# Kernel tuning notes

Measured on AMD Instinct MI355X. Metric: run time of the kernel, lower is better.

Reference implementation:

```python
import jax, jax.numpy as jnp
import numpy as np

B, CIN, H, W = 32, 64, 128, 128
HID, OUT, E, S, R = 64, 64, 8, 2, 16
TOP_K = 2
TEMP = 2.0
BN_EPS = 1e-5


def setup_inputs() -> dict:
    key = jax.random.key(0)
    ks = jax.random.split(key, 16)
    sc = lambda fan: 1.0 / np.sqrt(fan)
    h2 = 2 * HID
    return {
        "x": jax.random.normal(ks[0], (B, CIN, H, W), jnp.float32),
        "fe_w": jax.random.normal(ks[1], (HID, CIN), jnp.float32) * sc(CIN),
        "fe_b": jnp.zeros((HID,), jnp.float32),
        "s_w": jax.random.normal(ks[2], (S, OUT, HID), jnp.float32) * sc(HID),
        "s_b": jnp.zeros((S, OUT), jnp.float32),
        "e_w": jax.random.normal(ks[3], (E, OUT, HID), jnp.float32) * sc(HID),
        "e_b": jnp.zeros((E, OUT), jnp.float32),
        "g1_w": jax.random.normal(ks[4], (h2, HID), jnp.float32) * sc(HID),
        "g1_b": jnp.zeros((h2,), jnp.float32),
        "bn1_g": jnp.ones((h2,), jnp.float32),
        "bn1_b": jnp.zeros((h2,), jnp.float32),
        "ca1_w": jax.random.normal(ks[5], (h2 // R, h2), jnp.float32) * sc(h2),
        "ca1_b": jnp.zeros((h2 // R,), jnp.float32),
        "ca2_w": jax.random.normal(ks[6], (h2, h2 // R), jnp.float32) * sc(h2 // R),
        "ca2_b": jnp.zeros((h2,), jnp.float32),
        "g2_w": jax.random.normal(ks[7], (HID, h2), jnp.float32) * sc(h2),
        "g2_b": jnp.zeros((HID,), jnp.float32),
        "bn2_g": jnp.ones((HID,), jnp.float32),
        "bn2_b": jnp.zeros((HID,), jnp.float32),
        "g3_w": jax.random.normal(ks[8], (E, HID), jnp.float32) * sc(HID),
        "g3_b": jnp.zeros((E,), jnp.float32),
    }


def _gelu(v):
    return jax.nn.gelu(v, approximate=False)


def _bn_eval(v, g, b):
    # BatchNorm eval mode with running_mean=0, running_var=1
    return v * (g / np.sqrt(1.0 + BN_EPS)) + b


def reference(x, fe_w, fe_b, s_w, s_b, e_w, e_b, g1_w, g1_b, bn1_g, bn1_b,
              ca1_w, ca1_b, ca2_w, ca2_b, g2_w, g2_b, bn2_g, bn2_b, g3_w, g3_b):
    # feature extractor: 1x1 conv + GELU
    features = _gelu(jnp.einsum('bchw,oc->bohw', x, fe_w) + fe_b[None, :, None, None])

    # shared experts: mean of S expert outputs (sum / S)
    shared = _gelu(jnp.einsum('bchw,soc->bsohw', features, s_w)
                   + s_b[None, :, :, None, None]).mean(axis=1)

    # gating on globally pooled features [B, HID]
    gf = features.mean(axis=(2, 3))
    h1 = _gelu(_bn_eval(gf @ g1_w.T + g1_b, bn1_g, bn1_b))  # [B, 2*HID]
    # ChannelAttention on 1x1 spatial: avg_pool == max_pool == identity
    att = _gelu(h1 @ ca1_w.T + ca1_b) @ ca2_w.T + ca2_b
    h1 = h1 * jax.nn.sigmoid(att + att)  # avg_out + max_out are identical
    hh = _gelu(_bn_eval(h1 @ g2_w.T + g2_b, bn2_g, bn2_b))  # [B, HID]
    scores = hh @ g3_w.T + g3_b  # [B, E]

    top_vals, top_idx = jax.lax.top_k(scores, TOP_K)
    top_w = jax.nn.softmax(top_vals / TEMP, axis=1)  # [B, TOP_K]
    # dense per-(sample, expert) weights
    dense_w = jnp.zeros((x.shape[0], E), scores.dtype).at[
        jnp.arange(x.shape[0])[:, None], top_idx].add(top_w)

    # all experts on full batch, then weighted accumulate (matches original loop)
    eo = _gelu(jnp.einsum('bchw,eoc->beohw', features, e_w)
               + e_b[None, :, :, None, None])  # [B, E, OUT, H, W]
    routed = jnp.einsum('beohw,be->bohw', eo, dense_w)

    return shared + routed
```

## Files before the change

kernel.cpp:

```cpp
#include <hip/hip_runtime.h>
#include <hip/hip_bf16.h>
#include <stdint.h>

#define HW 16384

typedef __bf16 bf16_t;
typedef bf16_t bf16x8 __attribute__((ext_vector_type(8)));
typedef float f32x4 __attribute__((ext_vector_type(4)));

__device__ __forceinline__ float gelu_f(float x) {
    float t = x * fmaf(x * x, 0.044715f, 1.0f);
    float e = __builtin_amdgcn_exp2f(-2.3022083f * t);
    return x * __builtin_amdgcn_rcpf(1.0f + e);
}

__device__ __forceinline__ uint32_t pk2(float a, float b) {
    union { bf16_t h[2]; uint32_t u; } z;
    z.h[0] = (bf16_t)a; z.h[1] = (bf16_t)b;
    return z.u;
}

__device__ __forceinline__ void load16_to_lds(const float* g, float* lds) {
    __builtin_amdgcn_global_load_lds(
        (const __attribute__((address_space(1))) uint32_t*)g,
        (__attribute__((address_space(3))) uint32_t*)lds, 16, 0, 0);
}

__device__ __forceinline__ bf16x8 frag8(const float* src) {
    float4 lo = ((const float4*)src)[0];
    float4 hi = ((const float4*)src)[1];
    bf16x8 r;
    r[0] = (bf16_t)lo.x; r[1] = (bf16_t)lo.y; r[2] = (bf16_t)lo.z; r[3] = (bf16_t)lo.w;
    r[4] = (bf16_t)hi.x; r[5] = (bf16_t)hi.y; r[6] = (bf16_t)hi.z; r[7] = (bf16_t)hi.w;
    return r;
}

__device__ __forceinline__ bf16x8 frag44(const float* a, const float* b) {
    float4 lo = *(const float4*)a;
    float4 hi = *(const float4*)b;
    bf16x8 r;
    r[0] = (bf16_t)lo.x; r[1] = (bf16_t)lo.y; r[2] = (bf16_t)lo.z; r[3] = (bf16_t)lo.w;
    r[4] = (bf16_t)hi.x; r[5] = (bf16_t)hi.y; r[6] = (bf16_t)hi.z; r[7] = (bf16_t)hi.w;
    return r;
}

__global__ __launch_bounds__(256, 3)
void k1_feat(const float* __restrict__ x, const float* __restrict__ fe_w,
             const float* __restrict__ fe_b, bf16_t* __restrict__ feat,
             float* __restrict__ gf_part) {
    __shared__ float xs[3][64 * 64];
    __shared__ float gf4[4][64];

    int tid = threadIdx.x;
    int lane = tid & 63;
    int wid = tid >> 6;
    int r16 = lane & 15;
    int g = lane >> 4;
    int b = blockIdx.x >> 5;
    int ss = blockIdx.x & 31;
    int p0 = ss * 512;

    bf16x8 A[4][2];
    f32x4 bias[4];
#pragma unroll
    for (int ot = 0; ot < 4; ++ot) {
#pragma unroll
        for (int kh = 0; kh < 2; ++kh)
            A[ot][kh] = frag8(fe_w + (ot * 16 + r16) * 64 + kh * 32 + g * 8);
#pragma unroll
        for (int r = 0; r < 4; ++r) bias[ot][r] = fe_b[ot * 16 + g * 4 + r];
    }
    asm volatile("" ::: "memory");

    int j16 = lane & 15;
    int rsub = lane >> 4;

    auto STAGE = [&](int buf, int i) {
#pragma unroll
        for (int s = 0; s < 4; ++s) {
            int c0 = wid * 16 + s * 4;
            int c = c0 + rsub;
            int gch = j16 ^ (((c >> 3) & 3) << 2);
            const float* gsrc = x + (size_t)(b * 64 + c) * HW + p0 + i * 64 + gch * 4;
            load16_to_lds(gsrc, &xs[buf][c0 * 64]);
        }
    };

    float gfp[4][4] = {};
    bf16_t* featb = feat + (size_t)b * HW * 64;
    int wb = 16 * (wid ^ g) + r16;

    auto COMPUTE = [&](int buf, int i) {
        bf16x8 B0, B1;
#pragma unroll
        for (int j = 0; j < 8; ++j) {
            B0[j] = (bf16_t)xs[buf][(g * 8 + j) * 64 + wb];
            B1[j] = (bf16_t)xs[buf][(32 + g * 8 + j) * 64 + wb];
        }
        int pg = p0 + i * 64 + wid * 16 + r16;
        float vals[4][4];
#pragma unroll
        for (int ot = 0; ot < 4; ++ot) {
            f32x4 y = {0.f, 0.f, 0.f, 0.f};
            y = __builtin_amdgcn_mfma_f32_16x16x32_bf16(A[ot][0], B0, y, 0, 0, 0);
            y = __builtin_amdgcn_mfma_f32_16x16x32_bf16(A[ot][1], B1, y, 0, 0, 0);
#pragma unroll
            for (int r = 0; r < 4; ++r) {
                float v = gelu_f(y[r] + bias[ot][r]);
                gfp[ot][r] += v;
                vals[ot][r] = v;
            }
        }
        uint4 lo, hi;
        lo.x = pk2(vals[0][0], vals[0][1]); lo.y = pk2(vals[0][2], vals[0][3]);
        lo.z = pk2(vals[1][0], vals[1][1]); lo.w = pk2(vals[1][2], vals[1][3]);
        hi.x = pk2(vals[2][0], vals[2][1]); hi.y = pk2(vals[2][2], vals[2][3]);
        hi.z = pk2(vals[3][0], vals[3][1]); hi.w = pk2(vals[3][2], vals[3][3]);
        uint4* dst = (uint4*)(featb + (size_t)pg * 64 + g * 16);
        dst[0] = lo;
        dst[1] = hi;
    };

    STAGE(0, 0); STAGE(1, 1); STAGE(2, 2);
    asm volatile("s_waitcnt vmcnt(8)" ::: "memory");
    __builtin_amdgcn_s_barrier();

#define K1_STEP(i, buf, VM, ...) \
    COMPUTE(buf, i); \
    asm volatile("s_waitcnt lgkmcnt(0)" ::: "memory"); \
    __builtin_amdgcn_s_barrier(); \
    __VA_ARGS__; \
    asm volatile("s_waitcnt " VM ::: "memory"); \
    __builtin_amdgcn_s_barrier();

    K1_STEP(0, 0, "vmcnt(10)", STAGE(0, 3))
    K1_STEP(1, 1, "vmcnt(12)", STAGE(1, 4))
    K1_STEP(2, 2, "vmcnt(12)", STAGE(2, 5))
    K1_STEP(3, 0, "vmcnt(12)", STAGE(0, 6))
    K1_STEP(4, 1, "vmcnt(12)", STAGE(1, 7))
    K1_STEP(5, 2, "vmcnt(8)")
    K1_STEP(6, 0, "vmcnt(4)")
    COMPUTE(1, 7);
#undef K1_STEP

#pragma unroll
    for (int ot = 0; ot < 4; ++ot)
#pragma unroll
        for (int r = 0; r < 4; ++r) {
            float v = gfp[ot][r];
            v += __shfl_xor(v, 1);
            v += __shfl_xor(v, 2);
            v += __shfl_xor(v, 4);
            v += __shfl_xor(v, 8);
            if (r16 == 0) gf4[wid][ot * 16 + g * 4 + r] = v;
        }
    __syncthreads();
    if (tid < 64)
        gf_part[(size_t)blockIdx.x * 64 + tid] =
            gf4[0][tid] + gf4[1][tid] + gf4[2][tid] + gf4[3][tid];
}

__global__ __launch_bounds__(256)
void k2_gate(const float* __restrict__ gf_part,
             const float* __restrict__ g1_w, const float* __restrict__ g1_b,
             const float* __restrict__ bn1_g, const float* __restrict__ bn1_b,
             const float* __restrict__ ca1_w, const float* __restrict__ ca1_b,
             const float* __restrict__ ca2_w, const float* __restrict__ ca2_b,
             const float* __restrict__ g2_w, const float* __restrict__ g2_b,
             const float* __restrict__ bn2_g, const float* __restrict__ bn2_b,
             const float* __restrict__ g3_w, const float* __restrict__ g3_b,
             int* __restrict__ gidx, float* __restrict__ gw) {
    __shared__ float w1t[128 * 65];
    __shared__ float wc1[8 * 129];
    __shared__ float wc2[128 * 9];
    __shared__ float w2t[64 * 129];
    __shared__ float w3[8 * 65];
    __shared__ float gf[64], h1[128], a1[8], hh[64], sc[8];
    const float R1 = 0.99999500003749969f;
    int tid = threadIdx.x;
    int b = blockIdx.x;

    for (int i = tid; i < 2048; i += 256) {
        float4 v = ((const float4*)g1_w)[i];
        float* d = w1t + (i >> 4) * 65 + (i & 15) * 4;
        d[0] = v.x; d[1] = v.y; d[2] = v.z; d[3] = v.w;
    }
    for (int i = tid; i < 2048; i += 256) {
        float4 v = ((const float4*)g2_w)[i];
        float* d = w2t + (i >> 5) * 129 + (i & 31) * 4;
        d[0] = v.x; d[1] = v.y; d[2] = v.z; d[3] = v.w;
    }
    if (tid < 256) {
        int i = tid;
        float4 v = ((const float4*)ca1_w)[i];
        float* d = wc1 + (i >> 5) * 129 + (i & 31) * 4;
        d[0] = v.x; d[1] = v.y; d[2] = v.z; d[3] = v.w;
    }
    if (tid < 256) {
        int i = tid;
        float4 v = ((const float4*)ca2_w)[i];
        float* d = wc2 + (i >> 1) * 9 + (i & 1) * 4;
        d[0] = v.x; d[1] = v.y; d[2] = v.z; d[3] = v.w;
    }
    if (tid < 128) {
        int i = tid;
        float4 v = ((const float4*)g3_w)[i];
        float* d = w3 + (i >> 4) * 65 + (i & 15) * 4;
        d[0] = v.x; d[1] = v.y; d[2] = v.z; d[3] = v.w;
    }
    if (tid < 64) {
        float s0 = 0.f, s1 = 0.f;
#pragma unroll
        for (int ssi = 0; ssi < 32; ssi += 2) {
            s0 += gf_part[(size_t)(b * 32 + ssi) * 64 + tid];
            s1 += gf_part[(size_t)(b * 32 + ssi + 1) * 64 + tid];
        }
        gf[tid] = (s0 + s1) * (1.0f / 16384.0f);
    }
    __syncthreads();

    if (tid < 128) {
        int j = tid;
        float s0 = 0.f, s1 = 0.f;
#pragma unroll 8
        for (int c = 0; c < 64; c += 2) {
            s0 += gf[c] * w1t[j * 65 + c];
            s1 += gf[c + 1] * w1t[j * 65 + c + 1];
        }
        float s = g1_b[j] + s0 + s1;
        s = s * (bn1_g[j] * R1) + bn1_b[j];
        h1[j] = gelu_f(s);
    }
    __syncthreads();
    if (tid < 8) {
        int j = tid;
        float s0 = 0.f, s1 = 0.f;
#pragma unroll 8
        for (int c = 0; c < 128; c += 2) {
            s0 += h1[c] * wc1[j * 129 + c];
            s1 += h1[c + 1] * wc1[j * 129 + c + 1];
        }
        a1[j] = gelu_f(ca1_b[j] + s0 + s1);
    }
    __syncthreads();
    if (tid < 128) {
        int j = tid;
        float s = ca2_b[j];
#pragma unroll
        for (int r = 0; r < 8; ++r) s += a1[r] * wc2[j * 9 + r];
        float e2 = __builtin_amdgcn_exp2f(-2.8853901f * s);
        h1[j] = h1[j] * __builtin_amdgcn_rcpf(1.0f + e2);
    }
    __syncthreads();
    if (tid < 64) {
        int j = tid;
        float s0 = 0.f, s1 = 0.f;
#pragma unroll 8
        for (int c = 0; c < 128; c += 2) {
            s0 += h1[c] * w2t[j * 129 + c];
            s1 += h1[c + 1] * w2t[j * 129 + c + 1];
        }
        float s = g2_b[j] + s0 + s1;
        s = s * (bn2_g[j] * R1) + bn2_b[j];
        hh[j] = gelu_f(s);
    }
    __syncthreads();
    if (tid < 8) {
        int j = tid;
        float s0 = 0.f, s1 = 0.f;
#pragma unroll 8
        for (int c = 0; c < 64; c += 2) {
            s0 += hh[c] * w3[j * 65 + c];
            s1 += hh[c + 1] * w3[j * 65 + c + 1];
        }
        sc[j] = g3_b[j] + s0 + s1;
    }
    __syncthreads();
    if (tid == 0) {
        float v0 = -1e30f, v1 = -1e30f;
        int i0 = 0, i1 = 0;
#pragma unroll
        for (int e = 0; e < 8; ++e) {
            float s = sc[e];
            if (s > v0) { v1 = v0; i1 = i0; v0 = s; i0 = e; }
            else if (s > v1) { v1 = s; i1 = e; }
        }
        float t = __builtin_amdgcn_exp2f(0.7213475f * (v1 - v0));
        float den = __builtin_amdgcn_rcpf(1.0f + t);
        gidx[b * 2] = i0; gidx[b * 2 + 1] = i1;
        gw[b * 2] = den; gw[b * 2 + 1] = t * den;
    }
}

__global__ __launch_bounds__(256, 4)
void k3_out(const bf16_t* __restrict__ feat, const float* __restrict__ s_w,
            const float* __restrict__ s_b, const float* __restrict__ e_w,
            const float* __restrict__ e_b, const int* __restrict__ gidx,
            const float* __restrict__ gw, float* __restrict__ out) {
    int tid = threadIdx.x;
    int lane = tid & 63, wid = tid >> 6;
    int r16 = lane & 15, g = lane >> 4;
    int b = blockIdx.x >> 5;
    int stripe = blockIdx.x & 31;

    int i0 = gidx[2 * b], i1 = gidx[2 * b + 1];
    float coef[4] = {0.5f, 0.5f, gw[2 * b], gw[2 * b + 1]};
    const float* Wm[4] = {s_w, s_w + 4096,
                          e_w + (size_t)i0 * 4096, e_w + (size_t)i1 * 4096};
    const float* Bv[4] = {s_b, s_b + 64, e_b + i0 * 64, e_b + i1 * 64};

    bf16x8 Wf[4][2];
    float bias[4];
    int row = wid * 16 + r16;
#pragma unroll
    for (int m = 0; m < 4; ++m) {
#pragma unroll
        for (int kh = 0; kh < 2; ++kh) {
            int base = (g & 1) * 32 + (kh * 2 + (g >> 1)) * 4;
            Wf[m][kh] = frag44(Wm[m] + row * 64 + base,
                               Wm[m] + row * 64 + base + 16);
        }
        bias[m] = Bv[m][row];
    }

    const uint4* fb = (const uint4*)(feat + (size_t)b * HW * 64);
    float* outb = out + ((size_t)b * 64 + row) * HW + stripe * 512;
    int pbase = stripe * 512 + r16;

    auto BODY = [&](int t, uint4 u0, uint4 u1) {
        bf16x8 F0 = __builtin_bit_cast(bf16x8, u0);
        bf16x8 F1 = __builtin_bit_cast(bf16x8, u1);
        f32x4 acc = {0.f, 0.f, 0.f, 0.f};
#pragma unroll
        for (int m = 0; m < 4; ++m) {
            f32x4 y = {0.f, 0.f, 0.f, 0.f};
            y = __builtin_amdgcn_mfma_f32_16x16x32_bf16(F0, Wf[m][0], y, 0, 0, 0);
            y = __builtin_amdgcn_mfma_f32_16x16x32_bf16(F1, Wf[m][1], y, 0, 0, 0);
#pragma unroll
            for (int r = 0; r < 4; ++r)
                acc[r] += coef[m] * gelu_f(y[r] + bias[m]);
        }
        float4 st = {acc[0], acc[1], acc[2], acc[3]};
        *(float4*)(outb + t * 16 + g * 4) = st;
    };

    uint4 u0 = fb[(size_t)pbase * 8 + g];
    uint4 u1 = fb[(size_t)pbase * 8 + 4 + g];
#pragma unroll 4
    for (int t = 0; t < 31; ++t) {
        uint4 n0 = fb[(size_t)(pbase + (t + 1) * 16) * 8 + g];
        uint4 n1 = fb[(size_t)(pbase + (t + 1) * 16) * 8 + 4 + g];
        BODY(t, u0, u1);
        u0 = n0; u1 = n1;
    }
    BODY(31, u0, u1);
}

extern "C" void kernel_launch(void* const* d_in, const int* in_sizes, int n_in,
                              void* d_out, int out_size, void* d_ws, size_t ws_size,
                              hipStream_t stream) {
    (void)in_sizes; (void)n_in; (void)out_size; (void)ws_size;
    const float* x     = (const float*)d_in[0];
    const float* fe_w  = (const float*)d_in[1];
    const float* fe_b  = (const float*)d_in[2];
    const float* s_w   = (const float*)d_in[3];
    const float* s_b   = (const float*)d_in[4];
    const float* e_w   = (const float*)d_in[5];
    const float* e_b   = (const float*)d_in[6];
    const float* g1_w  = (const float*)d_in[7];
    const float* g1_b  = (const float*)d_in[8];
    const float* bn1_g = (const float*)d_in[9];
    const float* bn1_b = (const float*)d_in[10];
    const float* ca1_w = (const float*)d_in[11];
    const float* ca1_b = (const float*)d_in[12];
    const float* ca2_w = (const float*)d_in[13];
    const float* ca2_b = (const float*)d_in[14];
    const float* g2_w  = (const float*)d_in[15];
    const float* g2_b  = (const float*)d_in[16];
    const float* bn2_g = (const float*)d_in[17];
    const float* bn2_b = (const float*)d_in[18];
    const float* g3_w  = (const float*)d_in[19];
    const float* g3_b  = (const float*)d_in[20];
    float* out = (float*)d_out;

    char* wsb = (char*)d_ws;
    bf16_t* feat   = (bf16_t*)wsb;
    float* gf_part = (float*)(wsb + 67108864);
    int* gidx      = (int*)(wsb + 67108864 + 262144);
    float* gwts    = (float*)(wsb + 67108864 + 262144 + 256);

    k1_feat<<<1024, 256, 0, stream>>>(x, fe_w, fe_b, feat, gf_part);
    k2_gate<<<32, 256, 0, stream>>>(gf_part, g1_w, g1_b, bn1_g, bn1_b, ca1_w, ca1_b,
                                    ca2_w, ca2_b, g2_w, g2_b, bn2_g, bn2_b, g3_w, g3_b,
                                    gidx, gwts);
    k3_out<<<1024, 256, 0, stream>>>(feat, s_w, s_b, e_w, e_b, gidx, gwts, out);
}
```

Before: 359.0 us.

## Split feature and output kernels into finer per-wave tiles without block barriers

k1 now gives each wave its own 32-pixel tile with a single direct global-to-LDS load and no block-wide barriers. This replaces the triple-buffered 512-pixel block pipeline and runs four times as many blocks. k3 halves its stripe to 256 pixels, doubling its grid, and unrolls its prefetch two steps deep. The gate kernel now reduces 128 partial sums per sample. The aim is more parallelism and less synchronisation stall, at the cost of losing load/compute overlap inside a block and writing more partial sums.

```diff
diff --git a/kernel.cpp b/kernel.cpp
--- a/kernel.cpp
+++ b/kernel.cpp
@@ -44,11 +44,11 @@
     return r;
 }
 
-__global__ __launch_bounds__(256, 3)
+__global__ __launch_bounds__(256, 4)
 void k1_feat(const float* __restrict__ x, const float* __restrict__ fe_w,
              const float* __restrict__ fe_b, bf16_t* __restrict__ feat,
              float* __restrict__ gf_part) {
-    __shared__ float xs[3][64 * 64];
+    __shared__ float xs[4][32 * 64];
     __shared__ float gf4[4][64];
 
     int tid = threadIdx.x;
@@ -56,9 +56,9 @@
     int wid = tid >> 6;
     int r16 = lane & 15;
     int g = lane >> 4;
-    int b = blockIdx.x >> 5;
-    int ss = blockIdx.x & 31;
-    int p0 = ss * 512;
+    int gtile = blockIdx.x * 4 + wid;
+    int b = gtile >> 9;
+    int p0 = (gtile & 511) * 32;
 
     bf16x8 A[4][2];
     f32x4 bias[4];
@@ -72,76 +72,81 @@
     }
     asm volatile("" ::: "memory");
 
-    int j16 = lane & 15;
-    int rsub = lane >> 4;
-
-    auto STAGE = [&](int buf, int i) {
-#pragma unroll
-        for (int s = 0; s < 4; ++s) {
-            int c0 = wid * 16 + s * 4;
-            int c = c0 + rsub;
-            int gch = j16 ^ (((c >> 3) & 3) << 2);
-            const float* gsrc = x + (size_t)(b * 64 + c) * HW + p0 + i * 64 + gch * 4;
-            load16_to_lds(gsrc, &xs[buf][c0 * 64]);
-        }
-    };
+    float* xw = &xs[wid][0];
+    {
+        int rl = lane >> 3;
+        int ch0 = lane & 7;
+#pragma unroll
+        for (int s = 0; s < 8; ++s) {
+            int row = s * 8 + rl;
+            int gch = ch0 ^ ((s & 3) << 1);
+            const float* gsrc = x + (size_t)(b * 64 + row) * HW + p0 + gch * 4;
+            load16_to_lds(gsrc, xw + s * 256);
+        }
+    }
+
+    int cm0 = ((((r16 >> 2) + 0) ^ (g << 1)) << 2) + (r16 & 3);
+    int cm1 = ((((r16 >> 2) + 4) ^ (g << 1)) << 2) + (r16 & 3);
 
     float gfp[4][4] = {};
     bf16_t* featb = feat + (size_t)b * HW * 64;
-    int wb = 16 * (wid ^ g) + r16;
-
-    auto COMPUTE = [&](int buf, int i) {
-        bf16x8 B0, B1;
+
+    asm volatile("s_waitcnt vmcnt(4)" ::: "memory");
+
+    f32x4 y0[4], y1[4];
+    {
+        bf16x8 B00, B10;
 #pragma unroll
         for (int j = 0; j < 8; ++j) {
-            B0[j] = (bf16_t)xs[buf][(g * 8 + j) * 64 + wb];
-            B1[j] = (bf16_t)xs[buf][(32 + g * 8 + j) * 64 + wb];
-        }
-        int pg = p0 + i * 64 + wid * 16 + r16;
+            int ro = (g * 8 + j) * 32;
+            B00[j] = (bf16_t)xw[ro + cm0];
+            B10[j] = (bf16_t)xw[ro + cm1];
+        }
+#pragma unroll
+        for (int ot = 0; ot < 4; ++ot) {
+            f32x4 z = {0.f, 0.f, 0.f, 0.f};
+            y0[ot] = __builtin_amdgcn_mfma_f32_16x16x32_bf16(A[ot][0], B00, z, 0, 0, 0);
+            y1[ot] = __builtin_amdgcn_mfma_f32_16x16x32_bf16(A[ot][0], B10, z, 0, 0, 0);
+        }
+    }
+    asm volatile("s_waitcnt vmcnt(0)" ::: "memory");
+    {
+        bf16x8 B01, B11;
+#pragma unroll
+        for (int j = 0; j < 8; ++j) {
+            int ro = (32 + g * 8 + j) * 32;
+            B01[j] = (bf16_t)xw[ro + cm0];
+            B11[j] = (bf16_t)xw[ro + cm1];
+        }
+#pragma unroll
+        for (int ot = 0; ot < 4; ++ot) {
+            y0[ot] = __builtin_amdgcn_mfma_f32_16x16x32_bf16(A[ot][1], B01, y0[ot], 0, 0, 0);
+            y1[ot] = __builtin_amdgcn_mfma_f32_16x16x32_bf16(A[ot][1], B11, y1[ot], 0, 0, 0);
+        }
+    }
+
+#pragma unroll
+    for (int a = 0; a < 2; ++a) {
+        f32x4* y = a ? y1 : y0;
         float vals[4][4];
 #pragma unroll
-        for (int ot = 0; ot < 4; ++ot) {
-            f32x4 y = {0.f, 0.f, 0.f, 0.f};
-            y = __builtin_amdgcn_mfma_f32_16x16x32_bf16(A[ot][0], B0, y, 0, 0, 0);
-            y = __builtin_amdgcn_mfma_f32_16x16x32_bf16(A[ot][1], B1, y, 0, 0, 0);
+        for (int ot = 0; ot < 4; ++ot)
 #pragma unroll
             for (int r = 0; r < 4; ++r) {
-                float v = gelu_f(y[r] + bias[ot][r]);
+                float v = gelu_f(y[ot][r] + bias[ot][r]);
                 gfp[ot][r] += v;
                 vals[ot][r] = v;
             }
-        }
         uint4 lo, hi;
         lo.x = pk2(vals[0][0], vals[0][1]); lo.y = pk2(vals[0][2], vals[0][3]);
         lo.z = pk2(vals[1][0], vals[1][1]); lo.w = pk2(vals[1][2], vals[1][3]);
         hi.x = pk2(vals[2][0], vals[2][1]); hi.y = pk2(vals[2][2], vals[2][3]);
         hi.z = pk2(vals[3][0], vals[3][1]); hi.w = pk2(vals[3][2], vals[3][3]);
-        uint4* dst = (uint4*)(featb + (size_t)pg * 64 + g * 16);
+        int px = p0 + a * 16 + r16;
+        uint4* dst = (uint4*)(featb + (size_t)px * 64 + g * 16);
         dst[0] = lo;
         dst[1] = hi;
-    };
-
-    STAGE(0, 0); STAGE(1, 1); STAGE(2, 2);
-    asm volatile("s_waitcnt vmcnt(8)" ::: "memory");
-    __builtin_amdgcn_s_barrier();
-
-#define K1_STEP(i, buf, VM, ...) \
-    COMPUTE(buf, i); \
-    asm volatile("s_waitcnt lgkmcnt(0)" ::: "memory"); \
-    __builtin_amdgcn_s_barrier(); \
-    __VA_ARGS__; \
-    asm volatile("s_waitcnt " VM ::: "memory"); \
-    __builtin_amdgcn_s_barrier();
-
-    K1_STEP(0, 0, "vmcnt(10)", STAGE(0, 3))
-    K1_STEP(1, 1, "vmcnt(12)", STAGE(1, 4))
-    K1_STEP(2, 2, "vmcnt(12)", STAGE(2, 5))
-    K1_STEP(3, 0, "vmcnt(12)", STAGE(0, 6))
-    K1_STEP(4, 1, "vmcnt(12)", STAGE(1, 7))
-    K1_STEP(5, 2, "vmcnt(8)")
-    K1_STEP(6, 0, "vmcnt(4)")
-    COMPUTE(1, 7);
-#undef K1_STEP
+    }
 
 #pragma unroll
     for (int ot = 0; ot < 4; ++ot)
@@ -209,13 +214,16 @@
         d[0] = v.x; d[1] = v.y; d[2] = v.z; d[3] = v.w;
     }
     if (tid < 64) {
-        float s0 = 0.f, s1 = 0.f;
-#pragma unroll
-        for (int ssi = 0; ssi < 32; ssi += 2) {
-            s0 += gf_part[(size_t)(b * 32 + ssi) * 64 + tid];
-            s1 += gf_part[(size_t)(b * 32 + ssi + 1) * 64 + tid];
-        }
-        gf[tid] = (s0 + s1) * (1.0f / 16384.0f);
+        float s0 = 0.f, s1 = 0.f, s2 = 0.f, s3 = 0.f;
+        const float* gp = gf_part + (size_t)b * 128 * 64 + tid;
+#pragma unroll 8
+        for (int i = 0; i < 128; i += 4) {
+            s0 += gp[(size_t)(i + 0) * 64];
+            s1 += gp[(size_t)(i + 1) * 64];
+            s2 += gp[(size_t)(i + 2) * 64];
+            s3 += gp[(size_t)(i + 3) * 64];
+        }
+        gf[tid] = ((s0 + s1) + (s2 + s3)) * (1.0f / 16384.0f);
     }
     __syncthreads();
 
@@ -300,8 +308,8 @@
     int tid = threadIdx.x;
     int lane = tid & 63, wid = tid >> 6;
     int r16 = lane & 15, g = lane >> 4;
-    int b = blockIdx.x >> 5;
-    int stripe = blockIdx.x & 31;
+    int b = blockIdx.x >> 6;
+    int stripe = blockIdx.x & 63;
 
     int i0 = gidx[2 * b], i1 = gidx[2 * b + 1];
     float coef[4] = {0.5f, 0.5f, gw[2 * b], gw[2 * b + 1]};
@@ -324,8 +332,8 @@
     }
 
     const uint4* fb = (const uint4*)(feat + (size_t)b * HW * 64);
-    float* outb = out + ((size_t)b * 64 + row) * HW + stripe * 512;
-    int pbase = stripe * 512 + r16;
+    float* outb = out + ((size_t)b * 64 + row) * HW + stripe * 256;
+    int pbase = stripe * 256 + r16;
 
     auto BODY = [&](int t, uint4 u0, uint4 u1) {
         bf16x8 F0 = __builtin_bit_cast(bf16x8, u0);
@@ -344,16 +352,21 @@
         *(float4*)(outb + t * 16 + g * 4) = st;
     };
 
-    uint4 u0 = fb[(size_t)pbase * 8 + g];
-    uint4 u1 = fb[(size_t)pbase * 8 + 4 + g];
-#pragma unroll 4
-    for (int t = 0; t < 31; ++t) {
-        uint4 n0 = fb[(size_t)(pbase + (t + 1) * 16) * 8 + g];
-        uint4 n1 = fb[(size_t)(pbase + (t + 1) * 16) * 8 + 4 + g];
-        BODY(t, u0, u1);
-        u0 = n0; u1 = n1;
-    }
-    BODY(31, u0, u1);
+    uint4 a0 = fb[(size_t)pbase * 8 + g];
+    uint4 a1 = fb[(size_t)pbase * 8 + 4 + g];
+    uint4 b0 = fb[(size_t)(pbase + 16) * 8 + g];
+    uint4 b1 = fb[(size_t)(pbase + 16) * 8 + 4 + g];
+#pragma unroll
+    for (int t = 0; t < 14; t += 2) {
+        uint4 n0 = fb[(size_t)(pbase + (t + 2) * 16) * 8 + g];
+        uint4 n1 = fb[(size_t)(pbase + (t + 2) * 16) * 8 + 4 + g];
+        BODY(t, a0, a1); a0 = n0; a1 = n1;
+        uint4 m0 = fb[(size_t)(pbase + (t + 3) * 16) * 8 + g];
+        uint4 m1 = fb[(size_t)(pbase + (t + 3) * 16) * 8 + 4 + g];
+        BODY(t + 1, b0, b1); b0 = m0; b1 = m1;
+    }
+    BODY(14, a0, a1);
+    BODY(15, b0, b1);
 }
 
 extern "C" void kernel_launch(void* const* d_in, const int* in_sizes, int n_in,
@@ -386,12 +399,12 @@
     char* wsb = (char*)d_ws;
     bf16_t* feat   = (bf16_t*)wsb;
     float* gf_part = (float*)(wsb + 67108864);
-    int* gidx      = (int*)(wsb + 67108864 + 262144);
-    float* gwts    = (float*)(wsb + 67108864 + 262144 + 256);
-
-    k1_feat<<<1024, 256, 0, stream>>>(x, fe_w, fe_b, feat, gf_part);
+    int* gidx      = (int*)(wsb + 67108864 + 1048576);
+    float* gwts    = (float*)(wsb + 67108864 + 1048576 + 256);
+
+    k1_feat<<<4096, 256, 0, stream>>>(x, fe_w, fe_b, feat, gf_part);
     k2_gate<<<32, 256, 0, stream>>>(gf_part, g1_w, g1_b, bn1_g, bn1_b, ca1_w, ca1_b,
                                     ca2_w, ca2_b, g2_w, g2_b, bn2_g, bn2_b, g3_w, g3_b,
                                     gidx, gwts);
-    k3_out<<<1024, 256, 0, stream>>>(feat, s_w, s_b, e_w, e_b, gidx, gwts, out);
-}
+    k3_out<<<2048, 256, 0, stream>>>(feat, s_w, s_b, e_w, e_b, gidx, gwts, out);
+}
```

Measured after the change: 343.0 us. 4.5% less time.
